# Optimization experiments

Hardware: AMD Instinct MI355X
Metric: run time of the kernel (lower is better)

## Reference

```python
import jax, jax.numpy as jnp
import numpy as np

N_HEADS = 4
N_GROUPS = 32
EPS = 1e-5


def setup_inputs() -> dict:
    key = jax.random.key(0)
    ks = jax.random.split(key, 6)
    c = 512
    x = jax.random.normal(ks[0], (4, c, 64, 64), dtype=jnp.float32)
    # conv1x1 weights ~ kaiming-ish scale
    s = 1.0 / np.sqrt(c)
    wq = jax.random.normal(ks[1], (c, c), dtype=jnp.float32) * s
    wk = jax.random.normal(ks[2], (c, c), dtype=jnp.float32) * s
    wv = jax.random.normal(ks[3], (c, c), dtype=jnp.float32) * s
    wp = jax.random.normal(ks[4], (c, c), dtype=jnp.float32) * s
    zeros = jnp.zeros((c,), dtype=jnp.float32)
    return {
        "x": x,
        "gn_w": jnp.ones((c,), dtype=jnp.float32), "gn_b": zeros,
        "wq": wq, "bq": zeros, "wk": wk, "bk": zeros,
        "wv": wv, "bv": zeros, "wp": wp, "bp": zeros,
    }


def _group_norm(x, w, b):
    bsz, c, h, wd = x.shape
    xg = x.reshape(bsz, N_GROUPS, c // N_GROUPS, h, wd)
    mean = xg.mean(axis=(2, 3, 4), keepdims=True)
    var = xg.var(axis=(2, 3, 4), keepdims=True)
    xg = (xg - mean) * jax.lax.rsqrt(var + EPS)
    x = xg.reshape(bsz, c, h, wd)
    return x * w[None, :, None, None] + b[None, :, None, None]


def _conv1x1(x, w, b):
    # x: (b,c,h,w), w: (out,in) -> (b,out,h,w)
    return jnp.einsum('bchw,oc->bohw', x, w) + b[None, :, None, None]


def reference(x, gn_w, gn_b, wq, bq, wk, bk, wv, bv, wp, bp):
    bsz, c, h, wd = x.shape
    hd = c // N_HEADS
    hw = h * wd
    x_n = _group_norm(x, gn_w, gn_b)
    q = _conv1x1(x_n, wq, bq)
    k = _conv1x1(x_n, wk, bk)
    v = _conv1x1(x_n, wv, bv)

    def to_heads(t):
        # (b,c,h,w) -> (b, n_heads, hw, head_dim)
        return t.reshape(bsz, N_HEADS, hd, hw).transpose(0, 1, 3, 2)

    q, k, v = to_heads(q), to_heads(k), to_heads(v)
    scale = hd ** (-0.5)
    attn = jnp.einsum('bhqd,bhkd->bhqk', q, k) * scale  # (b,H,hw,hw)
    attn = jax.nn.softmax(attn, axis=-1)
    out = jnp.einsum('bhqk,bhkd->bhqd', attn, v)
    out = out.transpose(0, 1, 3, 2).reshape(bsz, c, h, wd)
    out = _conv1x1(out, wp, bp)
    return x + out
```

## Files before the change

kernel.cpp:

```cpp
#include <hip/hip_runtime.h>
#include <math.h>

typedef __attribute__((ext_vector_type(8))) short short8;
typedef __attribute__((ext_vector_type(4))) float floatx4;
typedef __attribute__((ext_vector_type(8))) unsigned short ushort8v;
typedef __attribute__((ext_vector_type(4))) unsigned short ushort4v;

#define HW 4096
#define CCH 512
#define NB 4
#define NH 4
#define HD 128

__device__ __forceinline__ unsigned short f2bf(float f) {
    union { float f; unsigned int u; } c; c.f = f;
    unsigned int u = c.u;
    u += 0x7FFFu + ((u >> 16) & 1u);
    return (unsigned short)(u >> 16);
}

__global__ void conv_w(const float* __restrict__ w0, const float* __restrict__ w1,
                       const float* __restrict__ w2, const float* __restrict__ w3,
                       unsigned short* __restrict__ dst) {
    const float* src = blockIdx.y == 0 ? w0 : blockIdx.y == 1 ? w1 : blockIdx.y == 2 ? w2 : w3;
    unsigned short* d = dst + (size_t)blockIdx.y * 262144;
    int i = blockIdx.x * 256 + threadIdx.x;
    float4 v = ((const float4*)src)[i];
    ushort4v o;
    o[0] = f2bf(v.x); o[1] = f2bf(v.y); o[2] = f2bf(v.z); o[3] = f2bf(v.w);
    ((ushort4v*)d)[i] = o;
}

__global__ void gn_stats(const float* __restrict__ x, float* __restrict__ stats) {
    int bg = blockIdx.x;
    int b = bg >> 5, g = bg & 31;
    const float4* p = (const float4*)(x + ((size_t)b * CCH + g * 16) * HW);
    float s = 0.f, ss = 0.f;
    for (int i = threadIdx.x; i < 16384; i += 256) {
        float4 v = p[i];
        s  += v.x + v.y + v.z + v.w;
        ss += v.x * v.x + v.y * v.y + v.z * v.z + v.w * v.w;
    }
    #pragma unroll
    for (int off = 32; off > 0; off >>= 1) {
        s  += __shfl_down(s, off, 64);
        ss += __shfl_down(ss, off, 64);
    }
    __shared__ float sm[4], sm2[4];
    int wid = threadIdx.x >> 6;
    if ((threadIdx.x & 63) == 0) { sm[wid] = s; sm2[wid] = ss; }
    __syncthreads();
    if (threadIdx.x == 0) {
        float ts = sm[0] + sm[1] + sm[2] + sm[3];
        float tss = sm2[0] + sm2[1] + sm2[2] + sm2[3];
        float mean = ts * (1.f / 65536.f);
        float var = tss * (1.f / 65536.f) - mean * mean;
        stats[bg * 2] = mean;
        stats[bg * 2 + 1] = rsqrtf(var + 1e-5f);
    }
}

__global__ void gn_apply(const float* __restrict__ x, const float* __restrict__ gnw,
                         const float* __restrict__ gnb, const float* __restrict__ stats,
                         unsigned short* __restrict__ xt) {
    int s = blockIdx.x * 256 + threadIdx.x;
    int g = blockIdx.y, b = blockIdx.z;
    float mean = stats[(b * 32 + g) * 2];
    float rstd = stats[(b * 32 + g) * 2 + 1];
    const float* xb = x + ((size_t)b * CCH + g * 16) * HW + s;
    unsigned short outv[16];
    #pragma unroll
    for (int cl = 0; cl < 16; cl++) {
        int c = g * 16 + cl;
        float v = xb[(size_t)cl * HW];
        v = (v - mean) * rstd * gnw[c] + gnb[c];
        outv[cl] = f2bf(v);
    }
    unsigned short* dst = xt + ((size_t)b * HW + s) * CCH + g * 16;
    *(ushort8v*)dst       = *(ushort8v*)&outv[0];
    *(ushort8v*)(dst + 8) = *(ushort8v*)&outv[8];
}

#define LDP 72
template <int MODE>
__global__ __launch_bounds__(256, 2) void gemm_nt(
    const unsigned short* __restrict__ A, long long aStride,
    const unsigned short* __restrict__ Bm, long long bStride,
    const float* __restrict__ bias, float scale,
    const float* __restrict__ resid, long long rStride,
    void* __restrict__ Cp, long long cStride, int ldc) {
    __shared__ unsigned short lA[128 * LDP];
    __shared__ unsigned short lB[128 * LDP];
    const int tid = threadIdx.x;
    const int lane = tid & 63;
    const int wid = tid >> 6;
    const int z = blockIdx.z;
    const unsigned short* Ab = A + (size_t)z * aStride + (size_t)blockIdx.x * 128 * 512;
    const unsigned short* Bb = Bm + (size_t)z * bStride + (size_t)blockIdx.y * 128 * 512;

    floatx4 acc[4][4];
    #pragma unroll
    for (int i = 0; i < 4; i++)
        #pragma unroll
        for (int j = 0; j < 4; j++) acc[i][j] = (floatx4)0.f;

    const int wm = (wid >> 1) * 64;
    const int wn = (wid & 1) * 64;
    const int l15 = lane & 15;
    const int l4 = lane >> 4;

    for (int k0 = 0; k0 < 512; k0 += 64) {
        #pragma unroll
        for (int i = 0; i < 4; i++) {
            int idx = i * 256 + tid;
            int row = idx >> 3;
            int kc = (idx & 7) * 8;
            *(ushort8v*)&lA[row * LDP + kc] = *(const ushort8v*)&Ab[(size_t)row * 512 + k0 + kc];
            *(ushort8v*)&lB[row * LDP + kc] = *(const ushort8v*)&Bb[(size_t)row * 512 + k0 + kc];
        }
        __syncthreads();
        #pragma unroll
        for (int kk = 0; kk < 2; kk++) {
            short8 af[4], bf[4];
            #pragma unroll
            for (int i = 0; i < 4; i++)
                af[i] = *(const short8*)&lA[(wm + i * 16 + l15) * LDP + kk * 32 + l4 * 8];
            #pragma unroll
            for (int j = 0; j < 4; j++)
                bf[j] = *(const short8*)&lB[(wn + j * 16 + l15) * LDP + kk * 32 + l4 * 8];
            #pragma unroll
            for (int i = 0; i < 4; i++)
                #pragma unroll
                for (int j = 0; j < 4; j++)
                    acc[i][j] = __builtin_amdgcn_mfma_f32_16x16x32_bf16(af[i], bf[j], acc[i][j], 0, 0, 0);
        }
        __syncthreads();
    }

    long long m0 = (long long)blockIdx.x * 128 + wm;
    long long n0 = (long long)blockIdx.y * 128 + wn;
    if (MODE == 0) {
        unsigned short* C = (unsigned short*)Cp + (size_t)z * cStride;
        #pragma unroll
        for (int i = 0; i < 4; i++)
            #pragma unroll
            for (int j = 0; j < 4; j++) {
                long long col = n0 + j * 16 + l15;
                float bv = bias[col];
                #pragma unroll
                for (int r = 0; r < 4; r++) {
                    long long row = m0 + i * 16 + l4 * 4 + r;
                    C[row * ldc + col] = f2bf((acc[i][j][r] + bv) * scale);
                }
            }
    } else if (MODE == 1) {
        float* C = (float*)Cp + (size_t)z * cStride;
        const float* R = resid + (size_t)z * rStride;
        #pragma unroll
        for (int i = 0; i < 4; i++)
            #pragma unroll
            for (int j = 0; j < 4; j++)
                #pragma unroll
                for (int r = 0; r < 4; r++) {
                    long long row = m0 + i * 16 + l4 * 4 + r;
                    long long col = n0 + j * 16 + l15;
                    C[row * ldc + col] = acc[i][j][r] + bias[row] + R[row * ldc + col];
                }
    } else {
        unsigned short* C = (unsigned short*)Cp + (size_t)z * cStride;
        #pragma unroll
        for (int i = 0; i < 4; i++)
            #pragma unroll
            for (int j = 0; j < 4; j++)
                #pragma unroll
                for (int r = 0; r < 4; r++) {
                    long long row = m0 + i * 16 + l4 * 4 + r;
                    long long col = n0 + j * 16 + l15;
                    C[row * ldc + col] = f2bf(acc[i][j][r] + bias[row]);
                }
    }
}

#define LQP 136
#define LTP 72
__global__ __launch_bounds__(256, 2) void attn_kern(
    const unsigned short* __restrict__ Qb, const unsigned short* __restrict__ Kb,
    const unsigned short* __restrict__ Vt, unsigned short* __restrict__ Ob) {
    __shared__ unsigned short lk[64 * LQP];
    __shared__ unsigned short lvt[128 * LTP];
    __shared__ unsigned short lp[128 * LTP];
    const int tid = threadIdx.x;
    const int lane = tid & 63;
    const int w = tid >> 6;
    const int l15 = lane & 15, l4 = lane >> 4;
    const int q0 = blockIdx.x * 128;
    const int h = blockIdx.y, b = blockIdx.z;
    const size_t headOff = (size_t)h * HD;
    const size_t batchRow = (size_t)b * HW;
    const unsigned short* VtB = Vt + ((size_t)b * CCH + headOff) * HW;

    short8 qf[2][4];
    #pragma unroll
    for (int i = 0; i < 2; i++)
        #pragma unroll
        for (int kk = 0; kk < 4; kk++)
            qf[i][kk] = *(const short8*)&Qb[(batchRow + q0 + w * 32 + i * 16 + l15) * 512
                                            + headOff + kk * 32 + l4 * 8];

    short8 onesf;
    {
        unsigned short o = (l15 == 0) ? (unsigned short)0x3F80 : (unsigned short)0;
        #pragma unroll
        for (int e = 0; e < 8; e++) onesf[e] = (short)o;
    }

    floatx4 acc_o[2][8];
    floatx4 acc_l[2];
    #pragma unroll
    for (int i = 0; i < 2; i++) {
        acc_l[i] = (floatx4)0.f;
        #pragma unroll
        for (int j = 0; j < 8; j++) acc_o[i][j] = (floatx4)0.f;
    }

    ushort8v kreg[4], vreg[4];
    #pragma unroll
    for (int i = 0; i < 4; i++) {
        int idx = i * 256 + tid;
        kreg[i] = *(const ushort8v*)&Kb[(batchRow + (idx >> 4)) * 512 + headOff + (idx & 15) * 8];
        vreg[i] = *(const ushort8v*)&VtB[(size_t)(idx >> 3) * HW + (idx & 7) * 8];
    }
    #pragma unroll
    for (int i = 0; i < 4; i++) {
        int idx = i * 256 + tid;
        *(ushort8v*)&lk[(idx >> 4) * LQP + (idx & 15) * 8] = kreg[i];
        *(ushort8v*)&lvt[(idx >> 3) * LTP + (idx & 7) * 8] = vreg[i];
    }
    __syncthreads();

    for (int kt = 0; kt < 64; kt++) {
        if (kt < 63) {
            int t0n = (kt + 1) * 64;
            #pragma unroll
            for (int i = 0; i < 4; i++) {
                int idx = i * 256 + tid;
                kreg[i] = *(const ushort8v*)&Kb[(batchRow + t0n + (idx >> 4)) * 512 + headOff + (idx & 15) * 8];
                vreg[i] = *(const ushort8v*)&VtB[(size_t)(idx >> 3) * HW + t0n + (idx & 7) * 8];
            }
        }

        floatx4 sa[2][4];
        #pragma unroll
        for (int i = 0; i < 2; i++)
            #pragma unroll
            for (int j = 0; j < 4; j++) sa[i][j] = (floatx4)0.f;
        #pragma unroll
        for (int kk = 0; kk < 4; kk++) {
            short8 bb[4];
            #pragma unroll
            for (int j = 0; j < 4; j++)
                bb[j] = *(const short8*)&lk[(j * 16 + l15) * LQP + kk * 32 + l4 * 8];
            #pragma unroll
            for (int i = 0; i < 2; i++)
                #pragma unroll
                for (int j = 0; j < 4; j++)
                    sa[i][j] = __builtin_amdgcn_mfma_f32_16x16x32_bf16(qf[i][kk], bb[j], sa[i][j], 0, 0, 0);
        }

        #pragma unroll
        for (int i = 0; i < 2; i++)
            #pragma unroll
            for (int j = 0; j < 4; j++)
                #pragma unroll
                for (int r = 0; r < 4; r++) {
                    float p = exp2f(sa[i][j][r]);
                    union { float f; unsigned int u; } c; c.f = p;
                    lp[(w * 32 + i * 16 + l4 * 4 + r) * LTP + j * 16 + l15] =
                        (unsigned short)((c.u + 0x8000u) >> 16);
                }

        #pragma unroll
        for (int ts = 0; ts < 2; ts++) {
            short8 pa[2];
            #pragma unroll
            for (int i = 0; i < 2; i++)
                pa[i] = *(const short8*)&lp[(w * 32 + i * 16 + l15) * LTP + ts * 32 + l4 * 8];
            #pragma unroll
            for (int j = 0; j < 8; j++) {
                short8 bb = *(const short8*)&lvt[(j * 16 + l15) * LTP + ts * 32 + l4 * 8];
                #pragma unroll
                for (int i = 0; i < 2; i++)
                    acc_o[i][j] = __builtin_amdgcn_mfma_f32_16x16x32_bf16(pa[i], bb, acc_o[i][j], 0, 0, 0);
            }
            #pragma unroll
            for (int i = 0; i < 2; i++)
                acc_l[i] = __builtin_amdgcn_mfma_f32_16x16x32_bf16(pa[i], onesf, acc_l[i], 0, 0, 0);
        }

        if (kt < 63) {
            __syncthreads();
            #pragma unroll
            for (int i = 0; i < 4; i++) {
                int idx = i * 256 + tid;
                *(ushort8v*)&lk[(idx >> 4) * LQP + (idx & 15) * 8] = kreg[i];
                *(ushort8v*)&lvt[(idx >> 3) * LTP + (idx & 7) * 8] = vreg[i];
            }
            __syncthreads();
        }
    }

    #pragma unroll
    for (int i = 0; i < 2; i++)
        #pragma unroll
        for (int r = 0; r < 4; r++) {
            float ls = __shfl(acc_l[i][r], lane & 48, 64);
            float rl = 1.f / ls;
            size_t row = batchRow + q0 + w * 32 + i * 16 + l4 * 4 + r;
            #pragma unroll
            for (int j = 0; j < 8; j++)
                Ob[row * 512 + headOff + j * 16 + l15] = f2bf(acc_o[i][j][r] * rl);
        }
}

extern "C" void kernel_launch(void* const* d_in, const int* in_sizes, int n_in,
                              void* d_out, int out_size, void* d_ws, size_t ws_size,
                              hipStream_t stream) {
    const float* x   = (const float*)d_in[0];
    const float* gnw = (const float*)d_in[1];
    const float* gnb = (const float*)d_in[2];
    const float* wq  = (const float*)d_in[3];
    const float* bq  = (const float*)d_in[4];
    const float* wk  = (const float*)d_in[5];
    const float* bk  = (const float*)d_in[6];
    const float* wv  = (const float*)d_in[7];
    const float* bv  = (const float*)d_in[8];
    const float* wp  = (const float*)d_in[9];
    const float* bp  = (const float*)d_in[10];
    float* out = (float*)d_out;

    const size_t NE = (size_t)NB * HW * CCH;
    unsigned short* ws16 = (unsigned short*)d_ws;
    unsigned short* XT = ws16;
    unsigned short* Qb = ws16 + NE;
    unsigned short* Kb = ws16 + 2 * NE;
    unsigned short* Vt = ws16 + 3 * NE;
    unsigned short* Wb = ws16 + 4 * NE;
    float* stats = (float*)(ws16 + 4 * NE + 4 * 262144);

    const float qscale = 0.08838834764831845f * 1.4426950408889634f;

    conv_w<<<dim3(256, 4), 256, 0, stream>>>(wq, wk, wv, wp, Wb);
    gn_stats<<<128, 256, 0, stream>>>(x, stats);
    gn_apply<<<dim3(16, 32, 4), 256, 0, stream>>>(x, gnw, gnb, stats, XT);

    gemm_nt<0><<<dim3(128, 4, 1), 256, 0, stream>>>(XT, 0, Wb + 0 * 262144, 0, bq, qscale, nullptr, 0, Qb, 0, 512);
    gemm_nt<0><<<dim3(128, 4, 1), 256, 0, stream>>>(XT, 0, Wb + 1 * 262144, 0, bk, 1.f, nullptr, 0, Kb, 0, 512);
    gemm_nt<2><<<dim3(4, 32, 4), 256, 0, stream>>>(Wb + 2 * 262144, 0, XT, (long long)HW * 512, bv, 1.f,
                                                   nullptr, 0, Vt, (long long)CCH * HW, HW);

    unsigned short* Ob = XT;
    attn_kern<<<dim3(32, NH, NB), 256, 0, stream>>>(Qb, Kb, Vt, Ob);

    gemm_nt<1><<<dim3(4, 32, 4), 256, 0, stream>>>(Wb + 3 * 262144, 0, Ob, (long long)HW * 512, bp, 1.f,
                                                   x, (long long)CCH * HW, out, (long long)CCH * HW, HW);
}
```

Baseline: 389.3 us.

## Keep softmax probabilities in registers by computing transposed scores in attention

The score MFMA is now computed as K·Qᵀ, so each lane's accumulator already matches the A-operand layout needed for the P·V MFMA. Probabilities are exponentiated and packed to bf16 in registers with v_cvt_pk_bf16_f32, which removes the LDS buffer for P and its store/load round trip. V fragments are loaded with a matching permuted key order, and the row sum uses an all-ones operand, so no shuffle is needed. The change also raises the launch-bounds occupancy target to 3 and adds s_setprio around the MFMA sections. The added register pressure could cause spills at the higher occupancy target.

```diff
diff --git a/kernel.cpp b/kernel.cpp
--- a/kernel.cpp
+++ b/kernel.cpp
@@ -183,12 +183,11 @@
 
 #define LQP 136
 #define LTP 72
-__global__ __launch_bounds__(256, 2) void attn_kern(
+__global__ __launch_bounds__(256, 3) void attn_kern(
     const unsigned short* __restrict__ Qb, const unsigned short* __restrict__ Kb,
     const unsigned short* __restrict__ Vt, unsigned short* __restrict__ Ob) {
     __shared__ unsigned short lk[64 * LQP];
     __shared__ unsigned short lvt[128 * LTP];
-    __shared__ unsigned short lp[128 * LTP];
     const int tid = threadIdx.x;
     const int lane = tid & 63;
     const int w = tid >> 6;
@@ -208,11 +207,8 @@
                                             + headOff + kk * 32 + l4 * 8];
 
     short8 onesf;
-    {
-        unsigned short o = (l15 == 0) ? (unsigned short)0x3F80 : (unsigned short)0;
-        #pragma unroll
-        for (int e = 0; e < 8; e++) onesf[e] = (short)o;
-    }
+    #pragma unroll
+    for (int e = 0; e < 8; e++) onesf[e] = (short)0x3F80;
 
     floatx4 acc_o[2][8];
     floatx4 acc_l[2];
@@ -239,6 +235,51 @@
     __syncthreads();
 
     for (int kt = 0; kt < 64; kt++) {
+        floatx4 sa[4][2];
+        #pragma unroll
+        for (int j = 0; j < 4; j++)
+            #pragma unroll
+            for (int i = 0; i < 2; i++) sa[j][i] = (floatx4)0.f;
+        __builtin_amdgcn_s_setprio(1);
+        #pragma unroll
+        for (int kk = 0; kk < 4; kk++) {
+            short8 kf[4];
+            #pragma unroll
+            for (int j = 0; j < 4; j++)
+                kf[j] = *(const short8*)&lk[(j * 16 + l15) * LQP + kk * 32 + l4 * 8];
+            #pragma unroll
+            for (int j = 0; j < 4; j++)
+                #pragma unroll
+                for (int i = 0; i < 2; i++)
+                    sa[j][i] = __builtin_amdgcn_mfma_f32_16x16x32_bf16(kf[j], qf[i][kk], sa[j][i], 0, 0, 0);
+        }
+        __builtin_amdgcn_s_setprio(0);
+
+        #pragma unroll
+        for (int j = 0; j < 4; j++)
+            #pragma unroll
+            for (int i = 0; i < 2; i++)
+                #pragma unroll
+                for (int r = 0; r < 4; r++)
+                    sa[j][i][r] = __builtin_amdgcn_exp2f(sa[j][i][r]);
+
+        short8 pa[2][2];
+        #pragma unroll
+        for (int i = 0; i < 2; i++)
+            #pragma unroll
+            for (int ts = 0; ts < 2; ts++) {
+                union { unsigned int u[4]; short8 s8; } pk;
+                asm("v_cvt_pk_bf16_f32 %0, %1, %2" : "=v"(pk.u[0])
+                    : "v"(sa[2 * ts][i][0]), "v"(sa[2 * ts][i][1]));
+                asm("v_cvt_pk_bf16_f32 %0, %1, %2" : "=v"(pk.u[1])
+                    : "v"(sa[2 * ts][i][2]), "v"(sa[2 * ts][i][3]));
+                asm("v_cvt_pk_bf16_f32 %0, %1, %2" : "=v"(pk.u[2])
+                    : "v"(sa[2 * ts + 1][i][0]), "v"(sa[2 * ts + 1][i][1]));
+                asm("v_cvt_pk_bf16_f32 %0, %1, %2" : "=v"(pk.u[3])
+                    : "v"(sa[2 * ts + 1][i][2]), "v"(sa[2 * ts + 1][i][3]));
+                pa[i][ts] = pk.s8;
+            }
+
         if (kt < 63) {
             int t0n = (kt + 1) * 64;
             #pragma unroll
@@ -249,53 +290,24 @@
             }
         }
 
-        floatx4 sa[2][4];
-        #pragma unroll
-        for (int i = 0; i < 2; i++)
-            #pragma unroll
-            for (int j = 0; j < 4; j++) sa[i][j] = (floatx4)0.f;
-        #pragma unroll
-        for (int kk = 0; kk < 4; kk++) {
-            short8 bb[4];
-            #pragma unroll
-            for (int j = 0; j < 4; j++)
-                bb[j] = *(const short8*)&lk[(j * 16 + l15) * LQP + kk * 32 + l4 * 8];
+        __builtin_amdgcn_s_setprio(1);
+        #pragma unroll
+        for (int ts = 0; ts < 2; ts++) {
             #pragma unroll
             for (int i = 0; i < 2; i++)
-                #pragma unroll
-                for (int j = 0; j < 4; j++)
-                    sa[i][j] = __builtin_amdgcn_mfma_f32_16x16x32_bf16(qf[i][kk], bb[j], sa[i][j], 0, 0, 0);
-        }
-
-        #pragma unroll
-        for (int i = 0; i < 2; i++)
-            #pragma unroll
-            for (int j = 0; j < 4; j++)
-                #pragma unroll
-                for (int r = 0; r < 4; r++) {
-                    float p = exp2f(sa[i][j][r]);
-                    union { float f; unsigned int u; } c; c.f = p;
-                    lp[(w * 32 + i * 16 + l4 * 4 + r) * LTP + j * 16 + l15] =
-                        (unsigned short)((c.u + 0x8000u) >> 16);
-                }
-
-        #pragma unroll
-        for (int ts = 0; ts < 2; ts++) {
-            short8 pa[2];
-            #pragma unroll
-            for (int i = 0; i < 2; i++)
-                pa[i] = *(const short8*)&lp[(w * 32 + i * 16 + l15) * LTP + ts * 32 + l4 * 8];
-            #pragma unroll
-            for (int j = 0; j < 8; j++) {
-                short8 bb = *(const short8*)&lvt[(j * 16 + l15) * LTP + ts * 32 + l4 * 8];
+                acc_l[i] = __builtin_amdgcn_mfma_f32_16x16x32_bf16(pa[i][ts], onesf, acc_l[i], 0, 0, 0);
+            #pragma unroll
+            for (int dj = 0; dj < 8; dj++) {
+                const unsigned short* vp = &lvt[(dj * 16 + l15) * LTP + ts * 32 + l4 * 4];
+                union { ushort4v h[2]; short8 s8; } vv;
+                vv.h[0] = *(const ushort4v*)vp;
+                vv.h[1] = *(const ushort4v*)(vp + 16);
                 #pragma unroll
                 for (int i = 0; i < 2; i++)
-                    acc_o[i][j] = __builtin_amdgcn_mfma_f32_16x16x32_bf16(pa[i], bb, acc_o[i][j], 0, 0, 0);
-            }
-            #pragma unroll
-            for (int i = 0; i < 2; i++)
-                acc_l[i] = __builtin_amdgcn_mfma_f32_16x16x32_bf16(pa[i], onesf, acc_l[i], 0, 0, 0);
-        }
+                    acc_o[i][dj] = __builtin_amdgcn_mfma_f32_16x16x32_bf16(pa[i][ts], vv.s8, acc_o[i][dj], 0, 0, 0);
+            }
+        }
+        __builtin_amdgcn_s_setprio(0);
 
         if (kt < 63) {
             __syncthreads();
@@ -313,12 +325,11 @@
     for (int i = 0; i < 2; i++)
         #pragma unroll
         for (int r = 0; r < 4; r++) {
-            float ls = __shfl(acc_l[i][r], lane & 48, 64);
-            float rl = 1.f / ls;
+            float rl = 1.f / acc_l[i][r];
             size_t row = batchRow + q0 + w * 32 + i * 16 + l4 * 4 + r;
             #pragma unroll
-            for (int j = 0; j < 8; j++)
-                Ob[row * 512 + headOff + j * 16 + l15] = f2bf(acc_o[i][j][r] * rl);
+            for (int dj = 0; dj < 8; dj++)
+                Ob[row * 512 + headOff + dj * 16 + l15] = f2bf(acc_o[i][dj][r] * rl);
         }
 }
 
```

Measured after the change: 495.9 us. 27.4% more time.
